# Performance work log

Measured on AMD Instinct MI355X. Metric: run time of the kernel, lower is better.

The kernel has to match this reference:

```python
import jax, jax.numpy as jnp
import numpy as np

ATTN = 512
HIDDEN = 1024
NUM_GENES = 2048
NUM_GF = 4


def setup_inputs() -> dict:
    key = jax.random.key(0)
    ks = jax.random.split(key, 8)
    s = 0.1
    return {
        "genes": jax.random.normal(ks[0], (32, NUM_GENES, NUM_GF), dtype=jnp.float32),
        "smiles": jax.random.normal(ks[1], (32, 2048, HIDDEN), dtype=jnp.float32),
        "w_num_gene_features": s * jax.random.normal(ks[2], (NUM_GF,), dtype=jnp.float32),
        "w_genes": s * jax.random.normal(ks[3], (NUM_GENES, ATTN), dtype=jnp.float32),
        "b_genes": s * jax.random.normal(ks[4], (ATTN,), dtype=jnp.float32),
        "w_smiles": s * jax.random.normal(ks[5], (HIDDEN, ATTN), dtype=jnp.float32),
        "b_smiles": s * jax.random.normal(ks[6], (ATTN,), dtype=jnp.float32),
        "v": s * jax.random.normal(ks[7], (ATTN,), dtype=jnp.float32),
    }


def reference(genes, smiles, w_num_gene_features, w_genes, b_genes, w_smiles, b_smiles, v):
    # genes: [B, G, F] -> collapse feature axis: [B, G]
    genes_collapsed = jnp.einsum("bgf,f->bg", genes, w_num_gene_features)
    # gene context projection: [B, A]
    x = jnp.einsum("bg,ga->ba", genes_collapsed, w_genes) + b_genes
    # smiles projection: [B, T, A]
    y = jnp.einsum("bth,ha->bta", smiles, w_smiles) + b_smiles
    h = jnp.tanh(x[:, None, :] + y)  # [B, T, A]
    scores = jnp.einsum("bta,a->bt", h, v)  # [B, T]
    alphas = jax.nn.softmax(scores, axis=-1)  # [B, T]
    # attention-weighted sum over sequence: [B, H]
    return jnp.einsum("bth,bt->bh", smiles, alphas)
```

## Files before the change

kernel.cpp:

```cpp
#include <hip/hip_runtime.h>


typedef __bf16 bf16_t;
typedef bf16_t bf16x8 __attribute__((ext_vector_type(8)));
typedef float f32x4 __attribute__((ext_vector_type(4)));

__device__ __forceinline__ unsigned short f32_to_bf16_rne(float f) {
    unsigned int u = __builtin_bit_cast(unsigned int, f);
    u = (u + 0x7FFFu + ((u >> 16) & 1u)) >> 16;
    return (unsigned short)u;
}

__device__ __forceinline__ float fast_tanh(float x) {
    float cx = fminf(fmaxf(x, -30.f), 30.f);
    float e = __expf(2.f * cx);
    return (e - 1.f) / (e + 1.f);
}

__global__ void k0b_pack(const float* __restrict__ w, unsigned short* __restrict__ Bp) {
    int bid  = blockIdx.x;
    int lane = threadIdx.x;
    int atile = bid >> 5, gks = bid & 31;
    int col = atile * 16 + (lane & 15);
    int k0  = gks * 32 + (lane >> 4) * 8;
    unsigned short us[8];
#pragma unroll
    for (int e = 0; e < 8; ++e)
        us[e] = f32_to_bf16_rne(w[(size_t)(k0 + e) * 512 + col]);
    *(uint4*)(Bp + (size_t)bid * 512 + lane * 8) = *(const uint4*)us;
}

__global__ void k1a_gc(const float4* __restrict__ genes, const float* __restrict__ wngf,
                       float* __restrict__ gc) {
    int i = blockIdx.x * 256 + threadIdx.x;
    float4 g = genes[i];
    gc[i] = g.x * wngf[0] + g.y * wngf[1] + g.z * wngf[2] + g.w * wngf[3];
}

__global__ void k1b_x(const float* __restrict__ gc, const float* __restrict__ wg,
                      float* __restrict__ x) {
    __shared__ float gcl[256];
    int bx = blockIdx.x;
    int b = bx >> 4, ah = (bx >> 3) & 1, gch = bx & 7;
    int g0 = gch * 256;
    gcl[threadIdx.x] = gc[b * 2048 + g0 + threadIdx.x];
    __syncthreads();
    int a = ah * 256 + threadIdx.x;
    float s = 0.f;
#pragma unroll 8
    for (int g = 0; g < 256; ++g) s += gcl[g] * wg[(size_t)(g0 + g) * 512 + a];
    atomicAdd(&x[b * 512 + a], s);
}

__global__ __launch_bounds__(512, 4) void k2_scores(
    const float* __restrict__ smiles,
    const unsigned short* __restrict__ Bp,
    const float* __restrict__ xraw,
    const float* __restrict__ b_genes,
    const float* __restrict__ b_smiles,
    const float* __restrict__ v,
    float* __restrict__ scores)
{
    __shared__ unsigned short A_lds[64 * 512];
    const int tid  = threadIdx.x;
    const int wave = tid >> 6;
    const int lane = tid & 63;
    const int l15  = lane & 15;
    const int l4   = lane >> 4;
    const int gm0  = blockIdx.x * 64;
    const int bidx = gm0 >> 11;
    const int wbase = wave * 64;

    const unsigned short* bpp = Bp + (size_t)(wave * 128) * 512 + lane * 8;

    const f32x4 zero4 = {0.f, 0.f, 0.f, 0.f};
    f32x4 acc[4][4];
#pragma unroll
    for (int mt = 0; mt < 4; ++mt)
#pragma unroll
        for (int nt = 0; nt < 4; ++nt)
            acc[mt][nt] = zero4;

    for (int kh = 0; kh < 2; ++kh) {
        __syncthreads();
        for (int half = 0; half < 4; ++half) {
            int u   = half * 1024 + tid * 2;
            int row = u >> 6;
            int kc  = u & 63;
            const float* src = smiles + (size_t)(gm0 + row) * 1024 + kh * 512 + kc * 8;
            float4 f0 = *(const float4*)(src);
            float4 f1 = *(const float4*)(src + 4);
            float4 f2 = *(const float4*)(src + 8);
            float4 f3 = *(const float4*)(src + 12);
            union { unsigned short us[8]; uint4 u4; } p0, p1;
            p0.us[0] = f32_to_bf16_rne(f0.x); p0.us[1] = f32_to_bf16_rne(f0.y);
            p0.us[2] = f32_to_bf16_rne(f0.z); p0.us[3] = f32_to_bf16_rne(f0.w);
            p0.us[4] = f32_to_bf16_rne(f1.x); p0.us[5] = f32_to_bf16_rne(f1.y);
            p0.us[6] = f32_to_bf16_rne(f1.z); p0.us[7] = f32_to_bf16_rne(f1.w);
            p1.us[0] = f32_to_bf16_rne(f2.x); p1.us[1] = f32_to_bf16_rne(f2.y);
            p1.us[2] = f32_to_bf16_rne(f2.z); p1.us[3] = f32_to_bf16_rne(f2.w);
            p1.us[4] = f32_to_bf16_rne(f3.x); p1.us[5] = f32_to_bf16_rne(f3.y);
            p1.us[6] = f32_to_bf16_rne(f3.z); p1.us[7] = f32_to_bf16_rne(f3.w);
            int swz = (row & 7) << 4;
            *(uint4*)((char*)A_lds + row * 1024 + ((kc * 16) ^ swz))        = p0.u4;
            *(uint4*)((char*)A_lds + row * 1024 + (((kc + 1) * 16) ^ swz))  = p1.u4;
        }
        __syncthreads();

#pragma unroll 4
        for (int ks = 0; ks < 16; ++ks) {
            int gks = kh * 16 + ks;
            bf16x8 af[4], bfb[4];
#pragma unroll
            for (int nt = 0; nt < 4; ++nt)
                bfb[nt] = *(const bf16x8*)(bpp + (nt * 32 + gks) * 512);
#pragma unroll
            for (int mt = 0; mt < 4; ++mt) {
                int row = mt * 16 + l15;
                int kl  = ks * 32 + l4 * 8;
                int byteoff = row * 1024 + ((kl * 2) ^ ((row & 7) << 4));
                af[mt] = *(const bf16x8*)((const char*)A_lds + byteoff);
            }
#pragma unroll
            for (int mt = 0; mt < 4; ++mt)
#pragma unroll
                for (int nt = 0; nt < 4; ++nt)
                    acc[mt][nt] = __builtin_amdgcn_mfma_f32_16x16x32_bf16(
                        af[mt], bfb[nt], acc[mt][nt], 0, 0, 0);
        }
    }

    float xbv[4], vv[4];
#pragma unroll
    for (int nt = 0; nt < 4; ++nt) {
        int a = wbase + nt * 16 + l15;
        xbv[nt] = xraw[bidx * 512 + a] + b_genes[a] + b_smiles[a];
        vv[nt]  = v[a];
    }
    float rs[4][4];
#pragma unroll
    for (int mt = 0; mt < 4; ++mt)
#pragma unroll
        for (int r = 0; r < 4; ++r)
            rs[mt][r] = 0.f;
#pragma unroll
    for (int mt = 0; mt < 4; ++mt)
#pragma unroll
        for (int nt = 0; nt < 4; ++nt)
#pragma unroll
            for (int r = 0; r < 4; ++r)
                rs[mt][r] += vv[nt] * fast_tanh(acc[mt][nt][r] + xbv[nt]);
#pragma unroll
    for (int mt = 0; mt < 4; ++mt)
#pragma unroll
        for (int r = 0; r < 4; ++r) {
            float s = rs[mt][r];
            s += __shfl_xor(s, 1);
            s += __shfl_xor(s, 2);
            s += __shfl_xor(s, 4);
            s += __shfl_xor(s, 8);
            rs[mt][r] = s;
        }
    if (l15 == 0) {
#pragma unroll
        for (int mt = 0; mt < 4; ++mt)
#pragma unroll
            for (int r = 0; r < 4; ++r)
                atomicAdd(&scores[gm0 + mt * 16 + l4 * 4 + r], rs[mt][r]);
    }
}

__global__ void k3_softmax(const float* __restrict__ scores, float* __restrict__ alphas) {
    __shared__ float redmax[4], redsum[4];
    int b = blockIdx.x, tid = threadIdx.x;
    int wave = tid >> 6;
    float sv[8];
    float mx = -1e30f;
#pragma unroll
    for (int i = 0; i < 8; ++i) {
        sv[i] = scores[b * 2048 + i * 256 + tid];
        mx = fmaxf(mx, sv[i]);
    }
#pragma unroll
    for (int m = 32; m >= 1; m >>= 1) mx = fmaxf(mx, __shfl_xor(mx, m));
    if ((tid & 63) == 0) redmax[wave] = mx;
    __syncthreads();
    mx = fmaxf(fmaxf(redmax[0], redmax[1]), fmaxf(redmax[2], redmax[3]));
    float sum = 0.f;
#pragma unroll
    for (int i = 0; i < 8; ++i) {
        sv[i] = __expf(sv[i] - mx);
        sum += sv[i];
    }
#pragma unroll
    for (int m = 32; m >= 1; m >>= 1) sum += __shfl_xor(sum, m);
    if ((tid & 63) == 0) redsum[wave] = sum;
    __syncthreads();
    sum = redsum[0] + redsum[1] + redsum[2] + redsum[3];
    float inv = 1.f / sum;
#pragma unroll
    for (int i = 0; i < 8; ++i) alphas[b * 2048 + i * 256 + tid] = sv[i] * inv;
}

__global__ void k4_out(const float* __restrict__ smiles,
                       const float* __restrict__ alphas,
                       float* __restrict__ out)
{
    int bx = blockIdx.x;
    int b  = bx >> 4;
    int tc = bx & 15;
    int h  = threadIdx.x * 4;
    const float* sb = smiles + ((size_t)b * 2048 + tc * 128) * 1024;
    const float* al = alphas + b * 2048 + tc * 128;
    float4 acc = {0.f, 0.f, 0.f, 0.f};
#pragma unroll 4
    for (int t = 0; t < 128; ++t) {
        float a = al[t];
        float4 sv = *(const float4*)(sb + (size_t)t * 1024 + h);
        acc.x += a * sv.x;
        acc.y += a * sv.y;
        acc.z += a * sv.z;
        acc.w += a * sv.w;
    }
    float* o = out + b * 1024 + h;
    atomicAdd(o + 0, acc.x);
    atomicAdd(o + 1, acc.y);
    atomicAdd(o + 2, acc.z);
    atomicAdd(o + 3, acc.w);
}

extern "C" void kernel_launch(void* const* d_in, const int* in_sizes, int n_in,
                              void* d_out, int out_size, void* d_ws, size_t ws_size,
                              hipStream_t stream) {
    const float* genes    = (const float*)d_in[0];
    const float* smiles   = (const float*)d_in[1];
    const float* w_ngf    = (const float*)d_in[2];
    const float* w_genes  = (const float*)d_in[3];
    const float* b_genes  = (const float*)d_in[4];
    const float* w_smiles = (const float*)d_in[5];
    const float* b_smiles = (const float*)d_in[6];
    const float* v        = (const float*)d_in[7];
    float* out = (float*)d_out;

    char* ws = (char*)d_ws;
    unsigned short* Bp = (unsigned short*)(ws);
    float* gc     = (float*)(ws + (1 << 20));
    float* x      = (float*)(ws + (1 << 20) + (256 << 10));
    float* scores = (float*)(ws + (1 << 20) + (320 << 10));
    float* alphas = (float*)(ws + (1 << 20) + (576 << 10));

    hipMemsetAsync(out, 0, (size_t)32 * 1024 * sizeof(float), stream);
    hipMemsetAsync(x, 0, (size_t)(64 + 256) * 1024, stream);

    k0b_pack<<<1024, 64, 0, stream>>>(w_smiles, Bp);
    k1a_gc<<<256, 256, 0, stream>>>((const float4*)genes, w_ngf, gc);
    k1b_x<<<512, 256, 0, stream>>>(gc, w_genes, x);
    k2_scores<<<1024, 512, 0, stream>>>(smiles, Bp, x, b_genes, b_smiles, v, scores);
    k3_softmax<<<32, 256, 0, stream>>>(scores, alphas);
    k4_out<<<512, 256, 0, stream>>>(smiles, alphas, out);
}
```

Baseline: 196.7 us.

## Double-buffer smiles K-tiles in LDS with register prefetch overlapping MFMA

```diff
diff --git a/kernel.cpp b/kernel.cpp
--- a/kernel.cpp
+++ b/kernel.cpp
@@ -61,7 +61,7 @@
     const float* __restrict__ v,
     float* __restrict__ scores)
 {
-    __shared__ unsigned short A_lds[64 * 512];
+    __shared__ unsigned short A_lds[2 * 64 * 128];
     const int tid  = threadIdx.x;
     const int wave = tid >> 6;
     const int lane = tid & 63;
@@ -73,6 +73,15 @@
 
     const unsigned short* bpp = Bp + (size_t)(wave * 128) * 512 + lane * 8;
 
+    const int srow = tid >> 3;
+    const int scol = (tid & 7) * 16;
+    const float* sptr = smiles + (size_t)(gm0 + srow) * 1024 + scol;
+    const int sswz = (srow & 7) << 4;
+    char* wr0 = (char*)A_lds + srow * 256 + (((tid & 7) * 32) ^ sswz);
+    char* wr1 = (char*)A_lds + srow * 256 + ((((tid & 7) * 32) + 16) ^ sswz);
+
+    float4 st0, st1, st2, st3;
+
     const f32x4 zero4 = {0.f, 0.f, 0.f, 0.f};
     f32x4 acc[4][4];
 #pragma unroll
@@ -81,54 +90,69 @@
         for (int nt = 0; nt < 4; ++nt)
             acc[mt][nt] = zero4;
 
-    for (int kh = 0; kh < 2; ++kh) {
+#define LOADREGS(kt)                                   \
+    {   const float* p = sptr + (kt) * 128;            \
+        st0 = *(const float4*)(p);                     \
+        st1 = *(const float4*)(p + 4);                 \
+        st2 = *(const float4*)(p + 8);                 \
+        st3 = *(const float4*)(p + 12); }
+
+#define CONVWRITE(buf)                                                     \
+    {   union { unsigned short us[8]; uint4 u4; } pa, pb;                  \
+        pa.us[0] = f32_to_bf16_rne(st0.x); pa.us[1] = f32_to_bf16_rne(st0.y); \
+        pa.us[2] = f32_to_bf16_rne(st0.z); pa.us[3] = f32_to_bf16_rne(st0.w); \
+        pa.us[4] = f32_to_bf16_rne(st1.x); pa.us[5] = f32_to_bf16_rne(st1.y); \
+        pa.us[6] = f32_to_bf16_rne(st1.z); pa.us[7] = f32_to_bf16_rne(st1.w); \
+        pb.us[0] = f32_to_bf16_rne(st2.x); pb.us[1] = f32_to_bf16_rne(st2.y); \
+        pb.us[2] = f32_to_bf16_rne(st2.z); pb.us[3] = f32_to_bf16_rne(st2.w); \
+        pb.us[4] = f32_to_bf16_rne(st3.x); pb.us[5] = f32_to_bf16_rne(st3.y); \
+        pb.us[6] = f32_to_bf16_rne(st3.z); pb.us[7] = f32_to_bf16_rne(st3.w); \
+        *(uint4*)(wr0 + (buf) * 16384) = pa.u4;                            \
+        *(uint4*)(wr1 + (buf) * 16384) = pb.u4; }
+
+#define COMPUTE(cur, kt)                                                      \
+    _Pragma("unroll")                                                         \
+    for (int ks4 = 0; ks4 < 4; ++ks4) {                                       \
+        int gks = (kt) * 4 + ks4;                                             \
+        bf16x8 af[4], bfb[4];                                                 \
+        _Pragma("unroll")                                                     \
+        for (int nt = 0; nt < 4; ++nt)                                        \
+            bfb[nt] = *(const bf16x8*)(bpp + (nt * 32 + gks) * 512);          \
+        _Pragma("unroll")                                                     \
+        for (int mt = 0; mt < 4; ++mt) {                                      \
+            int row = mt * 16 + l15;                                          \
+            int byteoff = (cur) * 16384 + row * 256 +                         \
+                          ((ks4 * 64 + l4 * 16) ^ ((row & 7) << 4));          \
+            af[mt] = *(const bf16x8*)((const char*)A_lds + byteoff);          \
+        }                                                                     \
+        __builtin_amdgcn_s_setprio(1);                                        \
+        _Pragma("unroll")                                                     \
+        for (int mt = 0; mt < 4; ++mt)                                        \
+            _Pragma("unroll")                                                 \
+            for (int nt = 0; nt < 4; ++nt)                                    \
+                acc[mt][nt] = __builtin_amdgcn_mfma_f32_16x16x32_bf16(        \
+                    af[mt], bfb[nt], acc[mt][nt], 0, 0, 0);                   \
+        __builtin_amdgcn_s_setprio(0);                                        \
+    }
+
+    LOADREGS(0);
+    CONVWRITE(0);
+    __syncthreads();
+
+    int cur = 0;
+#pragma unroll 1
+    for (int kt = 0; kt < 7; ++kt) {
+        LOADREGS(kt + 1);
+        COMPUTE(cur, kt);
+        CONVWRITE(cur ^ 1);
         __syncthreads();
-        for (int half = 0; half < 4; ++half) {
-            int u   = half * 1024 + tid * 2;
-            int row = u >> 6;
-            int kc  = u & 63;
-            const float* src = smiles + (size_t)(gm0 + row) * 1024 + kh * 512 + kc * 8;
-            float4 f0 = *(const float4*)(src);
-            float4 f1 = *(const float4*)(src + 4);
-            float4 f2 = *(const float4*)(src + 8);
-            float4 f3 = *(const float4*)(src + 12);
-            union { unsigned short us[8]; uint4 u4; } p0, p1;
-            p0.us[0] = f32_to_bf16_rne(f0.x); p0.us[1] = f32_to_bf16_rne(f0.y);
-            p0.us[2] = f32_to_bf16_rne(f0.z); p0.us[3] = f32_to_bf16_rne(f0.w);
-            p0.us[4] = f32_to_bf16_rne(f1.x); p0.us[5] = f32_to_bf16_rne(f1.y);
-            p0.us[6] = f32_to_bf16_rne(f1.z); p0.us[7] = f32_to_bf16_rne(f1.w);
-            p1.us[0] = f32_to_bf16_rne(f2.x); p1.us[1] = f32_to_bf16_rne(f2.y);
-            p1.us[2] = f32_to_bf16_rne(f2.z); p1.us[3] = f32_to_bf16_rne(f2.w);
-            p1.us[4] = f32_to_bf16_rne(f3.x); p1.us[5] = f32_to_bf16_rne(f3.y);
-            p1.us[6] = f32_to_bf16_rne(f3.z); p1.us[7] = f32_to_bf16_rne(f3.w);
-            int swz = (row & 7) << 4;
-            *(uint4*)((char*)A_lds + row * 1024 + ((kc * 16) ^ swz))        = p0.u4;
-            *(uint4*)((char*)A_lds + row * 1024 + (((kc + 1) * 16) ^ swz))  = p1.u4;
-        }
-        __syncthreads();
-
-#pragma unroll 4
-        for (int ks = 0; ks < 16; ++ks) {
-            int gks = kh * 16 + ks;
-            bf16x8 af[4], bfb[4];
-#pragma unroll
-            for (int nt = 0; nt < 4; ++nt)
-                bfb[nt] = *(const bf16x8*)(bpp + (nt * 32 + gks) * 512);
-#pragma unroll
-            for (int mt = 0; mt < 4; ++mt) {
-                int row = mt * 16 + l15;
-                int kl  = ks * 32 + l4 * 8;
-                int byteoff = row * 1024 + ((kl * 2) ^ ((row & 7) << 4));
-                af[mt] = *(const bf16x8*)((const char*)A_lds + byteoff);
-            }
-#pragma unroll
-            for (int mt = 0; mt < 4; ++mt)
-#pragma unroll
-                for (int nt = 0; nt < 4; ++nt)
-                    acc[mt][nt] = __builtin_amdgcn_mfma_f32_16x16x32_bf16(
-                        af[mt], bfb[nt], acc[mt][nt], 0, 0, 0);
-        }
-    }
+        cur ^= 1;
+    }
+    COMPUTE(cur, 7);
+
+#undef LOADREGS
+#undef CONVWRITE
+#undef COMPUTE
 
     float xbv[4], vv[4];
 #pragma unroll
```

After: 162.5 us. -17.4%, faster.

## Double-buffer smiles tiles via async global-to-LDS loads and split k4 finer

Applied to the files above, without the earlier changes.

```diff
diff --git a/kernel.cpp b/kernel.cpp
--- a/kernel.cpp
+++ b/kernel.cpp
@@ -16,6 +16,11 @@
     float e = __expf(2.f * cx);
     return (e - 1.f) / (e + 1.f);
 }
+
+#define GLL16(g, l)                                                        \
+    __builtin_amdgcn_global_load_lds(                                      \
+        (const __attribute__((address_space(1))) void*)(g),                \
+        (__attribute__((address_space(3))) void*)(l), 16, 0, 0)
 
 __global__ void k0b_pack(const float* __restrict__ w, unsigned short* __restrict__ Bp) {
     int bid  = blockIdx.x;
@@ -61,7 +66,7 @@
     const float* __restrict__ v,
     float* __restrict__ scores)
 {
-    __shared__ unsigned short A_lds[64 * 512];
+    __shared__ char A_lds[2 * 64 * 512];
     const int tid  = threadIdx.x;
     const int wave = tid >> 6;
     const int lane = tid & 63;
@@ -81,54 +86,63 @@
         for (int nt = 0; nt < 4; ++nt)
             acc[mt][nt] = zero4;
 
-    for (int kh = 0; kh < 2; ++kh) {
+#define STAGE(buf, kt)                                                          \
+    _Pragma("unroll")                                                           \
+    for (int i = 0; i < 4; ++i) {                                               \
+        int row = wave * 8 + i * 2 + (lane >> 5);                               \
+        int cc  = (lane & 31) ^ (row & 7);                                      \
+        const float* g = smiles + (size_t)(gm0 + row) * 1024 + (kt) * 128 + cc * 4; \
+        char* l = A_lds + (buf) * 32768 + wave * 4096 + i * 1024;               \
+        GLL16(g, l);                                                            \
+    }
+
+#define COMPUTE(cur, kt)                                                        \
+    _Pragma("unroll")                                                           \
+    for (int ks4 = 0; ks4 < 4; ++ks4) {                                         \
+        int gks = (kt) * 4 + ks4;                                               \
+        bf16x8 af[4], bfb[4];                                                   \
+        _Pragma("unroll")                                                       \
+        for (int nt = 0; nt < 4; ++nt)                                          \
+            bfb[nt] = *(const bf16x8*)(bpp + (nt * 32 + gks) * 512);            \
+        _Pragma("unroll")                                                       \
+        for (int mt = 0; mt < 4; ++mt) {                                        \
+            int row = mt * 16 + l15;                                            \
+            int sw  = (row & 7) << 4;                                           \
+            int base = (cur) * 32768 + row * 512;                               \
+            int off  = ks4 * 128 + l4 * 32;                                     \
+            f32x4 x0 = *(const f32x4*)(A_lds + base + (off ^ sw));              \
+            f32x4 x1 = *(const f32x4*)(A_lds + base + ((off + 16) ^ sw));       \
+            bf16x8 a;                                                           \
+            a[0] = (__bf16)x0[0]; a[1] = (__bf16)x0[1];                         \
+            a[2] = (__bf16)x0[2]; a[3] = (__bf16)x0[3];                         \
+            a[4] = (__bf16)x1[0]; a[5] = (__bf16)x1[1];                         \
+            a[6] = (__bf16)x1[2]; a[7] = (__bf16)x1[3];                         \
+            af[mt] = a;                                                         \
+        }                                                                       \
+        __builtin_amdgcn_s_setprio(1);                                          \
+        _Pragma("unroll")                                                       \
+        for (int mt = 0; mt < 4; ++mt)                                          \
+            _Pragma("unroll")                                                   \
+            for (int nt = 0; nt < 4; ++nt)                                      \
+                acc[mt][nt] = __builtin_amdgcn_mfma_f32_16x16x32_bf16(          \
+                    af[mt], bfb[nt], acc[mt][nt], 0, 0, 0);                     \
+        __builtin_amdgcn_s_setprio(0);                                          \
+    }
+
+    STAGE(0, 0);
+    __syncthreads();
+
+    int cur = 0;
+#pragma unroll 1
+    for (int kt = 0; kt < 8; ++kt) {
+        if (kt < 7) STAGE(cur ^ 1, kt + 1);
+        COMPUTE(cur, kt);
         __syncthreads();
-        for (int half = 0; half < 4; ++half) {
-            int u   = half * 1024 + tid * 2;
-            int row = u >> 6;
-            int kc  = u & 63;
-            const float* src = smiles + (size_t)(gm0 + row) * 1024 + kh * 512 + kc * 8;
-            float4 f0 = *(const float4*)(src);
-            float4 f1 = *(const float4*)(src + 4);
-            float4 f2 = *(const float4*)(src + 8);
-            float4 f3 = *(const float4*)(src + 12);
-            union { unsigned short us[8]; uint4 u4; } p0, p1;
-            p0.us[0] = f32_to_bf16_rne(f0.x); p0.us[1] = f32_to_bf16_rne(f0.y);
-            p0.us[2] = f32_to_bf16_rne(f0.z); p0.us[3] = f32_to_bf16_rne(f0.w);
-            p0.us[4] = f32_to_bf16_rne(f1.x); p0.us[5] = f32_to_bf16_rne(f1.y);
-            p0.us[6] = f32_to_bf16_rne(f1.z); p0.us[7] = f32_to_bf16_rne(f1.w);
-            p1.us[0] = f32_to_bf16_rne(f2.x); p1.us[1] = f32_to_bf16_rne(f2.y);
-            p1.us[2] = f32_to_bf16_rne(f2.z); p1.us[3] = f32_to_bf16_rne(f2.w);
-            p1.us[4] = f32_to_bf16_rne(f3.x); p1.us[5] = f32_to_bf16_rne(f3.y);
-            p1.us[6] = f32_to_bf16_rne(f3.z); p1.us[7] = f32_to_bf16_rne(f3.w);
-            int swz = (row & 7) << 4;
-            *(uint4*)((char*)A_lds + row * 1024 + ((kc * 16) ^ swz))        = p0.u4;
-            *(uint4*)((char*)A_lds + row * 1024 + (((kc + 1) * 16) ^ swz))  = p1.u4;
-        }
-        __syncthreads();
-
-#pragma unroll 4
-        for (int ks = 0; ks < 16; ++ks) {
-            int gks = kh * 16 + ks;
-            bf16x8 af[4], bfb[4];
-#pragma unroll
-            for (int nt = 0; nt < 4; ++nt)
-                bfb[nt] = *(const bf16x8*)(bpp + (nt * 32 + gks) * 512);
-#pragma unroll
-            for (int mt = 0; mt < 4; ++mt) {
-                int row = mt * 16 + l15;
-                int kl  = ks * 32 + l4 * 8;
-                int byteoff = row * 1024 + ((kl * 2) ^ ((row & 7) << 4));
-                af[mt] = *(const bf16x8*)((const char*)A_lds + byteoff);
-            }
-#pragma unroll
-            for (int mt = 0; mt < 4; ++mt)
-#pragma unroll
-                for (int nt = 0; nt < 4; ++nt)
-                    acc[mt][nt] = __builtin_amdgcn_mfma_f32_16x16x32_bf16(
-                        af[mt], bfb[nt], acc[mt][nt], 0, 0, 0);
-        }
-    }
+        cur ^= 1;
+    }
+
+#undef STAGE
+#undef COMPUTE
 
     float xbv[4], vv[4];
 #pragma unroll
@@ -207,14 +221,14 @@
                        float* __restrict__ out)
 {
     int bx = blockIdx.x;
-    int b  = bx >> 4;
-    int tc = bx & 15;
+    int b  = bx >> 5;
+    int tc = bx & 31;
     int h  = threadIdx.x * 4;
-    const float* sb = smiles + ((size_t)b * 2048 + tc * 128) * 1024;
-    const float* al = alphas + b * 2048 + tc * 128;
+    const float* sb = smiles + ((size_t)b * 2048 + tc * 64) * 1024;
+    const float* al = alphas + b * 2048 + tc * 64;
     float4 acc = {0.f, 0.f, 0.f, 0.f};
 #pragma unroll 4
-    for (int t = 0; t < 128; ++t) {
+    for (int t = 0; t < 64; ++t) {
         float a = al[t];
         float4 sv = *(const float4*)(sb + (size_t)t * 1024 + h);
         acc.x += a * sv.x;
@@ -257,5 +271,5 @@
     k1b_x<<<512, 256, 0, stream>>>(gc, w_genes, x);
     k2_scores<<<1024, 512, 0, stream>>>(smiles, Bp, x, b_genes, b_smiles, v, scores);
     k3_softmax<<<32, 256, 0, stream>>>(scores, alphas);
-    k4_out<<<512, 256, 0, stream>>>(smiles, alphas, out);
-}
+    k4_out<<<1024, 256, 0, stream>>>(smiles, alphas, out);
+}
```

New measurement: 183.0 us. -7.0%, faster.
